# Kernel optimization log

Hardware: AMD Instinct MI355X
Metric: run time of the kernel (lower is better)

The kernel has to match this reference:

```python
import jax, jax.numpy as jnp
import numpy as np

B, S, D, F, E = 4, 2048, 512, 2048, 8  # batch, seq, d_model, d_ff, n_experts


def setup_inputs() -> dict:
    key = jax.random.key(0)
    k = jax.random.split(key, 5)
    x = jax.random.normal(k[0], (B, S, D), dtype=jnp.float32)
    Ws = jax.random.normal(k[1], (D, E), dtype=jnp.float32) * 0.02  # router weight
    bs = jnp.zeros((E,), dtype=jnp.float32)
    W1 = jax.random.normal(k[2], (E, D, F), dtype=jnp.float32) * 0.02
    b1 = jnp.zeros((E, F), dtype=jnp.float32)
    W2 = jax.random.normal(k[3], (E, F, D), dtype=jnp.float32) * 0.02
    b2 = jnp.zeros((E, D), dtype=jnp.float32)
    return {"x": x, "Ws": Ws, "bs": bs, "W1": W1, "b1": b1, "W2": W2, "b2": b2}


def reference(x, Ws, bs, W1, b1, W2, b2):
    # x: [B, S, D]. The torch module permutes in and permutes back, so the
    # batch/seq layout is preserved end to end; flatten to tokens [T, D].
    Bb, Ss, Dd = x.shape
    xt = x.reshape(-1, Dd)                       # [T, D]
    logits = xt @ Ws + bs                        # [T, E]
    probs = jax.nn.softmax(logits, axis=-1)
    prob_max = jnp.max(probs, axis=-1)           # [T] top-1 routing prob
    routes = jnp.argmax(probs, axis=-1)          # [T] expert ids
    onehot = jax.nn.one_hot(routes, W1.shape[0], dtype=xt.dtype)  # [T, E]

    # Per-expert FFN (eval mode: dropout is identity). drop_tokens=False, so
    # every token is processed by its routed expert. Dense dispatch: each
    # expert runs on all tokens, combine selects the routed output per token.
    def expert_ffn(w1, bb1, w2, bb2):
        h = jax.nn.gelu(xt @ w1 + bb1, approximate=False)  # [T, F] exact GELU (nn.GELU default)
        return h @ w2 + bb2                                # [T, D]

    y = jax.vmap(expert_ffn)(W1, b1, W2, b2)     # [E, T, D]
    out = jnp.einsum("te,etd->td", onehot, y)    # combine (scatter of routed outputs)
    out = out * prob_max[:, None]                # is_scale_prob=True
    return out.reshape(Bb, Ss, Dd)
```

## Files before the change

kernel.cpp:

```cpp
#include <hip/hip_runtime.h>
#include <hip/hip_fp16.h>
#include <cmath>

#define Tn 8192
#define Dn 512
#define Fn 2048
#define En 8

typedef _Float16 f16x8 __attribute__((ext_vector_type(8)));
typedef _Float16 f16x4 __attribute__((ext_vector_type(4)));
typedef float f32x4 __attribute__((ext_vector_type(4)));

#define MAXTILES 136

__device__ __forceinline__ void gload16(const void* g, void* l) {
    __builtin_amdgcn_global_load_lds(
        (const __attribute__((address_space(1))) unsigned int*)g,
        (__attribute__((address_space(3))) unsigned int*)l, 16, 0, 0);
}

__device__ __forceinline__ float fast_gelu(float v) {
    float z = fabsf(v) * 0.70710678118654752f;
    float t = 1.0f / fmaf(0.3275911f, z, 1.0f);
    float p = t * fmaf(t, fmaf(t, fmaf(t, fmaf(t, 1.061405429f, -1.453152027f),
                                       1.421413741f), -0.284496736f), 0.254829592f);
    float e = __expf(-z * z);
    float erfa = fmaf(-p, e, 1.0f);
    float phi = 0.5f + copysignf(0.5f * erfa, v);
    return v * phi;
}

__global__ __launch_bounds__(256) void router_kernel(
    const float* __restrict__ x, const float* __restrict__ Ws,
    const float* __restrict__ bs, _Float16* __restrict__ x16,
    int* __restrict__ route, float* __restrict__ scale,
    int* __restrict__ poslocal, int* __restrict__ blockCounts)
{
    __shared__ int hist[8];
    const int tid = threadIdx.x;
    if (tid < 8) hist[tid] = 0;
    __syncthreads();

    const int lane = tid & 63;
    const int w = tid >> 6;
    const int tokBase = blockIdx.x * 32 + w * 8;

    float wreg[8][8];
#pragma unroll
    for (int j = 0; j < 4; ++j) {
        const float4* p = reinterpret_cast<const float4*>(Ws + (4 * lane + j) * En);
        float4 a = p[0], b = p[1];
        wreg[j][0] = a.x; wreg[j][1] = a.y; wreg[j][2] = a.z; wreg[j][3] = a.w;
        wreg[j][4] = b.x; wreg[j][5] = b.y; wreg[j][6] = b.z; wreg[j][7] = b.w;
    }
#pragma unroll
    for (int j = 0; j < 4; ++j) {
        const float4* p = reinterpret_cast<const float4*>(Ws + (256 + 4 * lane + j) * En);
        float4 a = p[0], b = p[1];
        wreg[4 + j][0] = a.x; wreg[4 + j][1] = a.y; wreg[4 + j][2] = a.z; wreg[4 + j][3] = a.w;
        wreg[4 + j][4] = b.x; wreg[4 + j][5] = b.y; wreg[4 + j][6] = b.z; wreg[4 + j][7] = b.w;
    }
    float bsv[8];
#pragma unroll
    for (int e = 0; e < 8; ++e) bsv[e] = bs[e];

    for (int it = 0; it < 8; ++it) {
        int t = tokBase + it;
        const float4* xr = reinterpret_cast<const float4*>(x + (size_t)t * Dn);
        float4 v0 = xr[lane];
        float4 v1 = xr[64 + lane];
        f16x4 h0, h1;
        h0[0] = (_Float16)v0.x; h0[1] = (_Float16)v0.y; h0[2] = (_Float16)v0.z; h0[3] = (_Float16)v0.w;
        h1[0] = (_Float16)v1.x; h1[1] = (_Float16)v1.y; h1[2] = (_Float16)v1.z; h1[3] = (_Float16)v1.w;
        *reinterpret_cast<f16x4*>(x16 + (size_t)t * Dn + 4 * lane) = h0;
        *reinterpret_cast<f16x4*>(x16 + (size_t)t * Dn + 256 + 4 * lane) = h1;

        float xv[8] = {v0.x, v0.y, v0.z, v0.w, v1.x, v1.y, v1.z, v1.w};
        float part[8];
#pragma unroll
        for (int e = 0; e < 8; ++e) part[e] = 0.f;
#pragma unroll
        for (int j = 0; j < 8; ++j)
#pragma unroll
            for (int e = 0; e < 8; ++e) part[e] = fmaf(xv[j], wreg[j][e], part[e]);
#pragma unroll
        for (int s = 32; s > 0; s >>= 1) {
#pragma unroll
            for (int e = 0; e < 8; ++e) part[e] += __shfl_xor(part[e], s);
        }
        if (lane == 0) {
            float lg[8];
            lg[0] = part[0] + bsv[0];
            float m = lg[0]; int am = 0;
#pragma unroll
            for (int e = 1; e < 8; ++e) {
                lg[e] = part[e] + bsv[e];
                if (lg[e] > m) { m = lg[e]; am = e; }
            }
            float sum = 0.f;
#pragma unroll
            for (int e = 0; e < 8; ++e) sum += expf(lg[e] - m);
            route[t] = am;
            scale[t] = 1.0f / sum;
            poslocal[t] = atomicAdd(&hist[am], 1);
        }
    }
    __syncthreads();
    if (tid < 8) blockCounts[blockIdx.x * 8 + tid] = hist[tid];
}

__global__ __launch_bounds__(256) void plan_kernel(
    const int* __restrict__ blockCounts,
    int* __restrict__ base,
    int* __restrict__ nTiles, int* __restrict__ tileExpert,
    int* __restrict__ tileBase, int* __restrict__ tileEnd)
{
    __shared__ int cnt[256 * 8];
    __shared__ int groupSum[32 * 8];
    __shared__ int groupBase[32 * 8];
    __shared__ int totals[8];
    __shared__ int offsets_s[8];
    const int tid = threadIdx.x;
    for (int i = tid; i < 2048; i += 256) cnt[i] = blockCounts[i];
    __syncthreads();
    const int e = tid & 7, g = tid >> 3;
    {
        int s = 0;
#pragma unroll
        for (int b = g * 8; b < g * 8 + 8; ++b) s += cnt[b * 8 + e];
        groupSum[g * 8 + e] = s;
    }
    __syncthreads();
    if (tid < 8) {
        int run = 0;
        for (int gg = 0; gg < 32; ++gg) {
            groupBase[gg * 8 + tid] = run;
            run += groupSum[gg * 8 + tid];
        }
        totals[tid] = run;
    }
    __syncthreads();
    if (tid == 0) {
        int off = 0, nt = 0;
        for (int ee = 0; ee < En; ++ee) {
            offsets_s[ee] = off;
            int c = totals[ee];
            int tiles = (c + 63) / 64;
            for (int r = 0; r < tiles; ++r) {
                tileExpert[nt] = ee;
                tileBase[nt] = off + r * 64;
                tileEnd[nt] = off + c;
                ++nt;
            }
            off += c;
        }
        *nTiles = nt;
    }
    __syncthreads();
    {
        int run = offsets_s[e] + groupBase[g * 8 + e];
#pragma unroll
        for (int b = g * 8; b < g * 8 + 8; ++b) {
            base[b * 8 + e] = run;
            run += cnt[b * 8 + e];
        }
    }
}

__global__ __launch_bounds__(256) void scatter_kernel(
    const int* __restrict__ route, const int* __restrict__ poslocal,
    const int* __restrict__ base, int* __restrict__ order)
{
    int t = blockIdx.x * 256 + threadIdx.x;
    if (t >= Tn) return;
    int e = route[t];
    int rb = t >> 5;
    order[base[rb * 8 + e] + poslocal[t]] = t;
}

__global__ __launch_bounds__(256) void transpose_cvt_kernel(
    const float* __restrict__ W1, const float* __restrict__ W2,
    _Float16* __restrict__ W1T, _Float16* __restrict__ W2T)
{
    __shared__ float tile[64][65];
    int bx = blockIdx.x;
    const float* in; _Float16* outp; int R, C, tR, tC;
    if (bx < 2048) {
        int e = bx >> 8, t = bx & 255;
        R = Dn; C = Fn; tR = t >> 5; tC = t & 31;
        in = W1 + (size_t)e * Dn * Fn;
        outp = W1T + (size_t)e * Dn * Fn;
    } else {
        int b2 = bx - 2048;
        int e = b2 >> 8, t = b2 & 255;
        R = Fn; C = Dn; tR = t >> 3; tC = t & 7;
        in = W2 + (size_t)e * Fn * Dn;
        outp = W2T + (size_t)e * Fn * Dn;
    }
    int r0 = tR * 64, c0 = tC * 64;
    int row = threadIdx.x >> 2, cq = threadIdx.x & 3;
#pragma unroll
    for (int i = 0; i < 4; ++i) {
        float4 v = *reinterpret_cast<const float4*>(in + (size_t)(r0 + row) * C + c0 + cq * 16 + i * 4);
        tile[row][cq * 16 + i * 4 + 0] = v.x;
        tile[row][cq * 16 + i * 4 + 1] = v.y;
        tile[row][cq * 16 + i * 4 + 2] = v.z;
        tile[row][cq * 16 + i * 4 + 3] = v.w;
    }
    __syncthreads();
    int col = threadIdx.x >> 2, rq = threadIdx.x & 3;
    f16x8 o0, o1;
#pragma unroll
    for (int i = 0; i < 8; ++i) o0[i] = (_Float16)tile[rq * 16 + i][col];
#pragma unroll
    for (int i = 0; i < 8; ++i) o1[i] = (_Float16)tile[rq * 16 + 8 + i][col];
    size_t base = (size_t)(c0 + col) * R + r0 + rq * 16;
    *reinterpret_cast<f16x8*>(outp + base) = o0;
    *reinterpret_cast<f16x8*>(outp + base + 8) = o1;
}

__global__ __launch_bounds__(64) void gemm1_kernel(
    const _Float16* __restrict__ x16, const _Float16* __restrict__ W1T,
    const float* __restrict__ b1, const int* __restrict__ order,
    const int* __restrict__ nTiles, const int* __restrict__ tileExpert,
    const int* __restrict__ tileBase, const int* __restrict__ tileEnd,
    _Float16* __restrict__ hbuf)
{
    __shared__ _Float16 As[64 * 64];
    __shared__ _Float16 Bs[64 * 64];
    const int bx = blockIdx.x;
    const int bt = (bx & 7) * 17 + (bx >> 3);
    if (bt >= *nTiles) return;
    const int e = tileExpert[bt], rowBase = tileBase[bt], rowEnd = tileEnd[bt];
    const int nBase = blockIdx.y * 64;
    const int lane = threadIdx.x;

    const int swc = ((lane & 7) ^ (lane >> 3)) * 8;
    const _Float16* Asrc[8];
    const _Float16* Bsrc[8];
#pragma unroll
    for (int p = 0; p < 8; ++p) {
        int r = p * 8 + (lane >> 3);
        int tok = order[min(rowBase + r, Tn - 1)];
        Asrc[p] = x16 + (size_t)tok * Dn + swc;
        Bsrc[p] = W1T + (size_t)e * Dn * Fn + (size_t)(nBase + r) * Dn + swc;
    }

#define STAGE1(kt) do {                                                  \
        _Pragma("unroll")                                                \
        for (int p = 0; p < 8; ++p) {                                    \
            gload16(Asrc[p] + (kt) * 64, As + (p * 64 + lane) * 8);      \
            gload16(Bsrc[p] + (kt) * 64, Bs + (p * 64 + lane) * 8);      \
        }                                                                \
    } while (0)

    const int fr = lane & 15;
    const int off0 = (((lane >> 4))     ^ (lane & 7)) * 8;
    const int off1 = ((4 + (lane >> 4)) ^ (lane & 7)) * 8;

    f32x4 acc[4][4];
#pragma unroll
    for (int m = 0; m < 4; ++m)
#pragma unroll
        for (int n = 0; n < 4; ++n) acc[m][n] = {0.f, 0.f, 0.f, 0.f};

    STAGE1(0);
    const int NKT = Dn / 64;
    for (int kt = 0; kt < NKT; ++kt) {
        asm volatile("s_waitcnt vmcnt(0)" ::: "memory");
        f16x8 af[4][2], bf[4][2];
#pragma unroll
        for (int m = 0; m < 4; ++m) {
            af[m][0] = *reinterpret_cast<const f16x8*>(As + (m * 16 + fr) * 64 + off0);
            af[m][1] = *reinterpret_cast<const f16x8*>(As + (m * 16 + fr) * 64 + off1);
        }
#pragma unroll
        for (int n = 0; n < 4; ++n) {
            bf[n][0] = *reinterpret_cast<const f16x8*>(Bs + (n * 16 + fr) * 64 + off0);
            bf[n][1] = *reinterpret_cast<const f16x8*>(Bs + (n * 16 + fr) * 64 + off1);
        }
        asm volatile("s_waitcnt lgkmcnt(0)" ::: "memory");
        if (kt + 1 < NKT) STAGE1(kt + 1);
        __builtin_amdgcn_s_setprio(1);
#pragma unroll
        for (int ks = 0; ks < 2; ++ks)
#pragma unroll
            for (int m = 0; m < 4; ++m)
#pragma unroll
                for (int n = 0; n < 4; ++n)
                    acc[m][n] = __builtin_amdgcn_mfma_f32_16x16x32_f16(af[m][ks], bf[n][ks], acc[m][n], 0, 0, 0);
        __builtin_amdgcn_s_setprio(0);
    }
#undef STAGE1

    float b1v[4];
#pragma unroll
    for (int n = 0; n < 4; ++n) b1v[n] = b1[(size_t)e * Fn + nBase + n * 16 + fr];
#pragma unroll
    for (int m = 0; m < 4; ++m) {
#pragma unroll
        for (int j = 0; j < 4; ++j) {
            int i = rowBase + m * 16 + (lane >> 4) * 4 + j;
            if (i < rowEnd) {
#pragma unroll
                for (int n = 0; n < 4; ++n) {
                    float g = fast_gelu(acc[m][n][j] + b1v[n]);
                    hbuf[(size_t)i * Fn + nBase + n * 16 + fr] = (_Float16)g;
                }
            }
        }
    }
}

__global__ __launch_bounds__(64) void gemm2_kernel(
    const _Float16* __restrict__ hbuf, const _Float16* __restrict__ W2T,
    const float* __restrict__ b2, const int* __restrict__ order,
    const float* __restrict__ scale,
    const int* __restrict__ nTiles, const int* __restrict__ tileExpert,
    const int* __restrict__ tileBase, const int* __restrict__ tileEnd,
    float* __restrict__ out)
{
    __shared__ _Float16 As[64 * 64];
    __shared__ _Float16 Bs[32 * 64];
    const int bx = blockIdx.x;
    const int bt = (bx & 7) * 17 + (bx >> 3);
    if (bt >= *nTiles) return;
    const int e = tileExpert[bt], rowBase = tileBase[bt], rowEnd = tileEnd[bt];
    const int nBase = blockIdx.y * 32;
    const int lane = threadIdx.x;

    const int swc = ((lane & 7) ^ (lane >> 3)) * 8;
    const _Float16* Asrc[8];
    const _Float16* Bsrc[4];
#pragma unroll
    for (int p = 0; p < 8; ++p) {
        int r = p * 8 + (lane >> 3);
        Asrc[p] = hbuf + (size_t)min(rowBase + r, Tn - 1) * Fn + swc;
    }
#pragma unroll
    for (int p = 0; p < 4; ++p) {
        int r = p * 8 + (lane >> 3);
        Bsrc[p] = W2T + (size_t)e * Fn * Dn + (size_t)(nBase + r) * Fn + swc;
    }

#define STAGE2(kt) do {                                                  \
        _Pragma("unroll")                                                \
        for (int p = 0; p < 8; ++p)                                      \
            gload16(Asrc[p] + (kt) * 64, As + (p * 64 + lane) * 8);      \
        _Pragma("unroll")                                                \
        for (int p = 0; p < 4; ++p)                                      \
            gload16(Bsrc[p] + (kt) * 64, Bs + (p * 64 + lane) * 8);      \
    } while (0)

    const int fr = lane & 15;
    const int off0 = (((lane >> 4))     ^ (lane & 7)) * 8;
    const int off1 = ((4 + (lane >> 4)) ^ (lane & 7)) * 8;

    f32x4 acc[4][2];
#pragma unroll
    for (int m = 0; m < 4; ++m)
#pragma unroll
        for (int n = 0; n < 2; ++n) acc[m][n] = {0.f, 0.f, 0.f, 0.f};

    STAGE2(0);
    const int NKT = Fn / 64;
    for (int kt = 0; kt < NKT; ++kt) {
        asm volatile("s_waitcnt vmcnt(0)" ::: "memory");
        f16x8 af[4][2], bf[2][2];
#pragma unroll
        for (int m = 0; m < 4; ++m) {
            af[m][0] = *reinterpret_cast<const f16x8*>(As + (m * 16 + fr) * 64 + off0);
            af[m][1] = *reinterpret_cast<const f16x8*>(As + (m * 16 + fr) * 64 + off1);
        }
#pragma unroll
        for (int n = 0; n < 2; ++n) {
            bf[n][0] = *reinterpret_cast<const f16x8*>(Bs + (n * 16 + fr) * 64 + off0);
            bf[n][1] = *reinterpret_cast<const f16x8*>(Bs + (n * 16 + fr) * 64 + off1);
        }
        asm volatile("s_waitcnt lgkmcnt(0)" ::: "memory");
        if (kt + 1 < NKT) STAGE2(kt + 1);
        __builtin_amdgcn_s_setprio(1);
#pragma unroll
        for (int ks = 0; ks < 2; ++ks)
#pragma unroll
            for (int m = 0; m < 4; ++m)
#pragma unroll
                for (int n = 0; n < 2; ++n)
                    acc[m][n] = __builtin_amdgcn_mfma_f32_16x16x32_f16(af[m][ks], bf[n][ks], acc[m][n], 0, 0, 0);
        __builtin_amdgcn_s_setprio(0);
    }
#undef STAGE2

    float b2v[2];
#pragma unroll
    for (int n = 0; n < 2; ++n) b2v[n] = b2[(size_t)e * Dn + nBase + n * 16 + fr];
#pragma unroll
    for (int m = 0; m < 4; ++m) {
#pragma unroll
        for (int j = 0; j < 4; ++j) {
            int i = rowBase + m * 16 + (lane >> 4) * 4 + j;
            if (i < rowEnd) {
                int tok = order[i];
                float s = scale[tok];
#pragma unroll
                for (int n = 0; n < 2; ++n)
                    out[(size_t)tok * Dn + nBase + n * 16 + fr] = (acc[m][n][j] + b2v[n]) * s;
            }
        }
    }
}

extern "C" void kernel_launch(void* const* d_in, const int* in_sizes, int n_in,
                              void* d_out, int out_size, void* d_ws, size_t ws_size,
                              hipStream_t stream) {
    const float* x  = (const float*)d_in[0];
    const float* Ws = (const float*)d_in[1];
    const float* bs = (const float*)d_in[2];
    const float* W1 = (const float*)d_in[3];
    const float* b1 = (const float*)d_in[4];
    const float* W2 = (const float*)d_in[5];
    const float* b2 = (const float*)d_in[6];
    float* out = (float*)d_out;

    char* ws = (char*)d_ws;
    int* nTiles      = (int*)(ws + 0);
    int* tileExpert  = (int*)(ws + 256);
    int* tileBase    = (int*)(ws + 1024);
    int* tileEnd     = (int*)(ws + 2048);
    int* route       = (int*)(ws + 4096);
    float* scale     = (float*)(ws + 4096 + 4 * Tn);
    int* poslocal    = (int*)(ws + 4096 + 8 * Tn);
    int* order       = (int*)(ws + 4096 + 12 * Tn);
    int* blockCounts = (int*)(ws + 4096 + 16 * Tn);
    int* base        = (int*)(ws + 4096 + 16 * Tn + 8192);
    _Float16* x16    = (_Float16*)(ws + (1 << 20));
    _Float16* W1T    = x16 + (size_t)Tn * Dn;
    _Float16* W2T    = W1T + (size_t)En * Dn * Fn;
    _Float16* hbuf   = W2T + (size_t)En * Fn * Dn;

    router_kernel<<<256, 256, 0, stream>>>(x, Ws, bs, x16, route, scale, poslocal, blockCounts);
    plan_kernel<<<1, 256, 0, stream>>>(blockCounts, base, nTiles, tileExpert, tileBase, tileEnd);
    scatter_kernel<<<Tn / 256, 256, 0, stream>>>(route, poslocal, base, order);
    transpose_cvt_kernel<<<4096, 256, 0, stream>>>(W1, W2, W1T, W2T);
    gemm1_kernel<<<dim3(MAXTILES, Fn / 64), 64, 0, stream>>>(
        x16, W1T, b1, order, nTiles, tileExpert, tileBase, tileEnd, hbuf);
    gemm2_kernel<<<dim3(MAXTILES, Dn / 32), 64, 0, stream>>>(
        hbuf, W2T, b2, order, scale, nTiles, tileExpert, tileBase, tileEnd, out);
}
```

Before: 129.0 us.

## Merge router with weight transpose and widen gemm2 N tile to 64

Folds the router and the weight transpose/convert into one prep kernel launch, with block index selecting the role. This removes a launch and lets the two independent workloads share the GPU. Separately, gemm2 now computes a 64x64 output tile per block instead of 64x32, which halves the number of times the A (hbuf) tile is reloaded. The cost is more accumulator registers per thread and fewer blocks in the gemm2 grid.

```diff
diff --git a/kernel.cpp b/kernel.cpp
--- a/kernel.cpp
+++ b/kernel.cpp
@@ -30,83 +30,125 @@
     return v * phi;
 }
 
-__global__ __launch_bounds__(256) void router_kernel(
+__global__ __launch_bounds__(256) void prep_kernel(
     const float* __restrict__ x, const float* __restrict__ Ws,
     const float* __restrict__ bs, _Float16* __restrict__ x16,
     int* __restrict__ route, float* __restrict__ scale,
-    int* __restrict__ poslocal, int* __restrict__ blockCounts)
+    int* __restrict__ poslocal, int* __restrict__ blockCounts,
+    const float* __restrict__ W1, const float* __restrict__ W2,
+    _Float16* __restrict__ W1T, _Float16* __restrict__ W2T)
 {
+    __shared__ float tilebuf[64][65];
     __shared__ int hist[8];
     const int tid = threadIdx.x;
-    if (tid < 8) hist[tid] = 0;
+
+    if (blockIdx.x < 256) {
+        if (tid < 8) hist[tid] = 0;
+        __syncthreads();
+
+        const int lane = tid & 63;
+        const int w = tid >> 6;
+        const int tokBase = blockIdx.x * 32 + w * 8;
+
+        float wreg[8][8];
+#pragma unroll
+        for (int j = 0; j < 4; ++j) {
+            const float4* p = reinterpret_cast<const float4*>(Ws + (4 * lane + j) * En);
+            float4 a = p[0], b = p[1];
+            wreg[j][0] = a.x; wreg[j][1] = a.y; wreg[j][2] = a.z; wreg[j][3] = a.w;
+            wreg[j][4] = b.x; wreg[j][5] = b.y; wreg[j][6] = b.z; wreg[j][7] = b.w;
+        }
+#pragma unroll
+        for (int j = 0; j < 4; ++j) {
+            const float4* p = reinterpret_cast<const float4*>(Ws + (256 + 4 * lane + j) * En);
+            float4 a = p[0], b = p[1];
+            wreg[4 + j][0] = a.x; wreg[4 + j][1] = a.y; wreg[4 + j][2] = a.z; wreg[4 + j][3] = a.w;
+            wreg[4 + j][4] = b.x; wreg[4 + j][5] = b.y; wreg[4 + j][6] = b.z; wreg[4 + j][7] = b.w;
+        }
+        float bsv[8];
+#pragma unroll
+        for (int e = 0; e < 8; ++e) bsv[e] = bs[e];
+
+        for (int it = 0; it < 8; ++it) {
+            int t = tokBase + it;
+            const float4* xr = reinterpret_cast<const float4*>(x + (size_t)t * Dn);
+            float4 v0 = xr[lane];
+            float4 v1 = xr[64 + lane];
+            f16x4 h0, h1;
+            h0[0] = (_Float16)v0.x; h0[1] = (_Float16)v0.y; h0[2] = (_Float16)v0.z; h0[3] = (_Float16)v0.w;
+            h1[0] = (_Float16)v1.x; h1[1] = (_Float16)v1.y; h1[2] = (_Float16)v1.z; h1[3] = (_Float16)v1.w;
+            *reinterpret_cast<f16x4*>(x16 + (size_t)t * Dn + 4 * lane) = h0;
+            *reinterpret_cast<f16x4*>(x16 + (size_t)t * Dn + 256 + 4 * lane) = h1;
+
+            float xv[8] = {v0.x, v0.y, v0.z, v0.w, v1.x, v1.y, v1.z, v1.w};
+            float part[8];
+#pragma unroll
+            for (int e = 0; e < 8; ++e) part[e] = 0.f;
+#pragma unroll
+            for (int j = 0; j < 8; ++j)
+#pragma unroll
+                for (int e = 0; e < 8; ++e) part[e] = fmaf(xv[j], wreg[j][e], part[e]);
+#pragma unroll
+            for (int s = 32; s > 0; s >>= 1) {
+#pragma unroll
+                for (int e = 0; e < 8; ++e) part[e] += __shfl_xor(part[e], s);
+            }
+            if (lane == 0) {
+                float lg[8];
+                lg[0] = part[0] + bsv[0];
+                float m = lg[0]; int am = 0;
+#pragma unroll
+                for (int e = 1; e < 8; ++e) {
+                    lg[e] = part[e] + bsv[e];
+                    if (lg[e] > m) { m = lg[e]; am = e; }
+                }
+                float sum = 0.f;
+#pragma unroll
+                for (int e = 0; e < 8; ++e) sum += expf(lg[e] - m);
+                route[t] = am;
+                scale[t] = 1.0f / sum;
+                poslocal[t] = atomicAdd(&hist[am], 1);
+            }
+        }
+        __syncthreads();
+        if (tid < 8) blockCounts[blockIdx.x * 8 + tid] = hist[tid];
+        return;
+    }
+
+    int bx = blockIdx.x - 256;
+    const float* in; _Float16* outp; int R, C, tR, tC;
+    if (bx < 2048) {
+        int e = bx >> 8, t = bx & 255;
+        R = Dn; C = Fn; tR = t >> 5; tC = t & 31;
+        in = W1 + (size_t)e * Dn * Fn;
+        outp = W1T + (size_t)e * Dn * Fn;
+    } else {
+        int b2 = bx - 2048;
+        int e = b2 >> 8, t = b2 & 255;
+        R = Fn; C = Dn; tR = t >> 3; tC = t & 7;
+        in = W2 + (size_t)e * Fn * Dn;
+        outp = W2T + (size_t)e * Fn * Dn;
+    }
+    int r0 = tR * 64, c0 = tC * 64;
+    int row = tid >> 2, cq = tid & 3;
+#pragma unroll
+    for (int i = 0; i < 4; ++i) {
+        float4 v = *reinterpret_cast<const float4*>(in + (size_t)(r0 + row) * C + c0 + cq * 16 + i * 4);
+        tilebuf[row][cq * 16 + i * 4 + 0] = v.x;
+        tilebuf[row][cq * 16 + i * 4 + 1] = v.y;
+        tilebuf[row][cq * 16 + i * 4 + 2] = v.z;
+        tilebuf[row][cq * 16 + i * 4 + 3] = v.w;
+    }
     __syncthreads();
-
-    const int lane = tid & 63;
-    const int w = tid >> 6;
-    const int tokBase = blockIdx.x * 32 + w * 8;
-
-    float wreg[8][8];
-#pragma unroll
-    for (int j = 0; j < 4; ++j) {
-        const float4* p = reinterpret_cast<const float4*>(Ws + (4 * lane + j) * En);
-        float4 a = p[0], b = p[1];
-        wreg[j][0] = a.x; wreg[j][1] = a.y; wreg[j][2] = a.z; wreg[j][3] = a.w;
-        wreg[j][4] = b.x; wreg[j][5] = b.y; wreg[j][6] = b.z; wreg[j][7] = b.w;
-    }
-#pragma unroll
-    for (int j = 0; j < 4; ++j) {
-        const float4* p = reinterpret_cast<const float4*>(Ws + (256 + 4 * lane + j) * En);
-        float4 a = p[0], b = p[1];
-        wreg[4 + j][0] = a.x; wreg[4 + j][1] = a.y; wreg[4 + j][2] = a.z; wreg[4 + j][3] = a.w;
-        wreg[4 + j][4] = b.x; wreg[4 + j][5] = b.y; wreg[4 + j][6] = b.z; wreg[4 + j][7] = b.w;
-    }
-    float bsv[8];
-#pragma unroll
-    for (int e = 0; e < 8; ++e) bsv[e] = bs[e];
-
-    for (int it = 0; it < 8; ++it) {
-        int t = tokBase + it;
-        const float4* xr = reinterpret_cast<const float4*>(x + (size_t)t * Dn);
-        float4 v0 = xr[lane];
-        float4 v1 = xr[64 + lane];
-        f16x4 h0, h1;
-        h0[0] = (_Float16)v0.x; h0[1] = (_Float16)v0.y; h0[2] = (_Float16)v0.z; h0[3] = (_Float16)v0.w;
-        h1[0] = (_Float16)v1.x; h1[1] = (_Float16)v1.y; h1[2] = (_Float16)v1.z; h1[3] = (_Float16)v1.w;
-        *reinterpret_cast<f16x4*>(x16 + (size_t)t * Dn + 4 * lane) = h0;
-        *reinterpret_cast<f16x4*>(x16 + (size_t)t * Dn + 256 + 4 * lane) = h1;
-
-        float xv[8] = {v0.x, v0.y, v0.z, v0.w, v1.x, v1.y, v1.z, v1.w};
-        float part[8];
-#pragma unroll
-        for (int e = 0; e < 8; ++e) part[e] = 0.f;
-#pragma unroll
-        for (int j = 0; j < 8; ++j)
-#pragma unroll
-            for (int e = 0; e < 8; ++e) part[e] = fmaf(xv[j], wreg[j][e], part[e]);
-#pragma unroll
-        for (int s = 32; s > 0; s >>= 1) {
-#pragma unroll
-            for (int e = 0; e < 8; ++e) part[e] += __shfl_xor(part[e], s);
-        }
-        if (lane == 0) {
-            float lg[8];
-            lg[0] = part[0] + bsv[0];
-            float m = lg[0]; int am = 0;
-#pragma unroll
-            for (int e = 1; e < 8; ++e) {
-                lg[e] = part[e] + bsv[e];
-                if (lg[e] > m) { m = lg[e]; am = e; }
-            }
-            float sum = 0.f;
-#pragma unroll
-            for (int e = 0; e < 8; ++e) sum += expf(lg[e] - m);
-            route[t] = am;
-            scale[t] = 1.0f / sum;
-            poslocal[t] = atomicAdd(&hist[am], 1);
-        }
-    }
-    __syncthreads();
-    if (tid < 8) blockCounts[blockIdx.x * 8 + tid] = hist[tid];
+    int col = tid >> 2, rq = tid & 3;
+    f16x8 o0, o1;
+#pragma unroll
+    for (int i = 0; i < 8; ++i) o0[i] = (_Float16)tilebuf[rq * 16 + i][col];
+#pragma unroll
+    for (int i = 0; i < 8; ++i) o1[i] = (_Float16)tilebuf[rq * 16 + 8 + i][col];
+    size_t base = (size_t)(c0 + col) * R + r0 + rq * 16;
+    *reinterpret_cast<f16x8*>(outp + base) = o0;
+    *reinterpret_cast<f16x8*>(outp + base + 8) = o1;
 }
 
 __global__ __launch_bounds__(256) void plan_kernel(
@@ -178,47 +220,6 @@
     order[base[rb * 8 + e] + poslocal[t]] = t;
 }
 
-__global__ __launch_bounds__(256) void transpose_cvt_kernel(
-    const float* __restrict__ W1, const float* __restrict__ W2,
-    _Float16* __restrict__ W1T, _Float16* __restrict__ W2T)
-{
-    __shared__ float tile[64][65];
-    int bx = blockIdx.x;
-    const float* in; _Float16* outp; int R, C, tR, tC;
-    if (bx < 2048) {
-        int e = bx >> 8, t = bx & 255;
-        R = Dn; C = Fn; tR = t >> 5; tC = t & 31;
-        in = W1 + (size_t)e * Dn * Fn;
-        outp = W1T + (size_t)e * Dn * Fn;
-    } else {
-        int b2 = bx - 2048;
-        int e = b2 >> 8, t = b2 & 255;
-        R = Fn; C = Dn; tR = t >> 3; tC = t & 7;
-        in = W2 + (size_t)e * Fn * Dn;
-        outp = W2T + (size_t)e * Fn * Dn;
-    }
-    int r0 = tR * 64, c0 = tC * 64;
-    int row = threadIdx.x >> 2, cq = threadIdx.x & 3;
-#pragma unroll
-    for (int i = 0; i < 4; ++i) {
-        float4 v = *reinterpret_cast<const float4*>(in + (size_t)(r0 + row) * C + c0 + cq * 16 + i * 4);
-        tile[row][cq * 16 + i * 4 + 0] = v.x;
-        tile[row][cq * 16 + i * 4 + 1] = v.y;
-        tile[row][cq * 16 + i * 4 + 2] = v.z;
-        tile[row][cq * 16 + i * 4 + 3] = v.w;
-    }
-    __syncthreads();
-    int col = threadIdx.x >> 2, rq = threadIdx.x & 3;
-    f16x8 o0, o1;
-#pragma unroll
-    for (int i = 0; i < 8; ++i) o0[i] = (_Float16)tile[rq * 16 + i][col];
-#pragma unroll
-    for (int i = 0; i < 8; ++i) o1[i] = (_Float16)tile[rq * 16 + 8 + i][col];
-    size_t base = (size_t)(c0 + col) * R + r0 + rq * 16;
-    *reinterpret_cast<f16x8*>(outp + base) = o0;
-    *reinterpret_cast<f16x8*>(outp + base + 8) = o1;
-}
-
 __global__ __launch_bounds__(64) void gemm1_kernel(
     const _Float16* __restrict__ x16, const _Float16* __restrict__ W1T,
     const float* __restrict__ b1, const int* __restrict__ order,
@@ -321,59 +322,54 @@
     float* __restrict__ out)
 {
     __shared__ _Float16 As[64 * 64];
-    __shared__ _Float16 Bs[32 * 64];
+    __shared__ _Float16 Bs[64 * 64];
     const int bx = blockIdx.x;
     const int bt = (bx & 7) * 17 + (bx >> 3);
     if (bt >= *nTiles) return;
     const int e = tileExpert[bt], rowBase = tileBase[bt], rowEnd = tileEnd[bt];
-    const int nBase = blockIdx.y * 32;
+    const int nBase = blockIdx.y * 64;
     const int lane = threadIdx.x;
 
     const int swc = ((lane & 7) ^ (lane >> 3)) * 8;
     const _Float16* Asrc[8];
-    const _Float16* Bsrc[4];
+    const _Float16* Bsrc[8];
 #pragma unroll
     for (int p = 0; p < 8; ++p) {
         int r = p * 8 + (lane >> 3);
         Asrc[p] = hbuf + (size_t)min(rowBase + r, Tn - 1) * Fn + swc;
-    }
-#pragma unroll
-    for (int p = 0; p < 4; ++p) {
-        int r = p * 8 + (lane >> 3);
         Bsrc[p] = W2T + (size_t)e * Fn * Dn + (size_t)(nBase + r) * Fn + swc;
     }
 
 #define STAGE2(kt) do {                                                  \
         _Pragma("unroll")                                                \
-        for (int p = 0; p < 8; ++p)                                      \
+        for (int p = 0; p < 8; ++p) {                                    \
             gload16(Asrc[p] + (kt) * 64, As + (p * 64 + lane) * 8);      \
-        _Pragma("unroll")                                                \
-        for (int p = 0; p < 4; ++p)                                      \
             gload16(Bsrc[p] + (kt) * 64, Bs + (p * 64 + lane) * 8);      \
+        }                                                                \
     } while (0)
 
     const int fr = lane & 15;
     const int off0 = (((lane >> 4))     ^ (lane & 7)) * 8;
     const int off1 = ((4 + (lane >> 4)) ^ (lane & 7)) * 8;
 
-    f32x4 acc[4][2];
+    f32x4 acc[4][4];
 #pragma unroll
     for (int m = 0; m < 4; ++m)
 #pragma unroll
-        for (int n = 0; n < 2; ++n) acc[m][n] = {0.f, 0.f, 0.f, 0.f};
+        for (int n = 0; n < 4; ++n) acc[m][n] = {0.f, 0.f, 0.f, 0.f};
 
     STAGE2(0);
     const int NKT = Fn / 64;
     for (int kt = 0; kt < NKT; ++kt) {
         asm volatile("s_waitcnt vmcnt(0)" ::: "memory");
-        f16x8 af[4][2], bf[2][2];
+        f16x8 af[4][2], bf[4][2];
 #pragma unroll
         for (int m = 0; m < 4; ++m) {
             af[m][0] = *reinterpret_cast<const f16x8*>(As + (m * 16 + fr) * 64 + off0);
             af[m][1] = *reinterpret_cast<const f16x8*>(As + (m * 16 + fr) * 64 + off1);
         }
 #pragma unroll
-        for (int n = 0; n < 2; ++n) {
+        for (int n = 0; n < 4; ++n) {
             bf[n][0] = *reinterpret_cast<const f16x8*>(Bs + (n * 16 + fr) * 64 + off0);
             bf[n][1] = *reinterpret_cast<const f16x8*>(Bs + (n * 16 + fr) * 64 + off1);
         }
@@ -385,15 +381,15 @@
 #pragma unroll
             for (int m = 0; m < 4; ++m)
 #pragma unroll
-                for (int n = 0; n < 2; ++n)
+                for (int n = 0; n < 4; ++n)
                     acc[m][n] = __builtin_amdgcn_mfma_f32_16x16x32_f16(af[m][ks], bf[n][ks], acc[m][n], 0, 0, 0);
         __builtin_amdgcn_s_setprio(0);
     }
 #undef STAGE2
 
-    float b2v[2];
-#pragma unroll
-    for (int n = 0; n < 2; ++n) b2v[n] = b2[(size_t)e * Dn + nBase + n * 16 + fr];
+    float b2v[4];
+#pragma unroll
+    for (int n = 0; n < 4; ++n) b2v[n] = b2[(size_t)e * Dn + nBase + n * 16 + fr];
 #pragma unroll
     for (int m = 0; m < 4; ++m) {
 #pragma unroll
@@ -403,7 +399,7 @@
                 int tok = order[i];
                 float s = scale[tok];
 #pragma unroll
-                for (int n = 0; n < 2; ++n)
+                for (int n = 0; n < 4; ++n)
                     out[(size_t)tok * Dn + nBase + n * 16 + fr] = (acc[m][n][j] + b2v[n]) * s;
             }
         }
@@ -438,12 +434,12 @@
     _Float16* W2T    = W1T + (size_t)En * Dn * Fn;
     _Float16* hbuf   = W2T + (size_t)En * Fn * Dn;
 
-    router_kernel<<<256, 256, 0, stream>>>(x, Ws, bs, x16, route, scale, poslocal, blockCounts);
+    prep_kernel<<<256 + 4096, 256, 0, stream>>>(x, Ws, bs, x16, route, scale, poslocal,
+                                                blockCounts, W1, W2, W1T, W2T);
     plan_kernel<<<1, 256, 0, stream>>>(blockCounts, base, nTiles, tileExpert, tileBase, tileEnd);
     scatter_kernel<<<Tn / 256, 256, 0, stream>>>(route, poslocal, base, order);
-    transpose_cvt_kernel<<<4096, 256, 0, stream>>>(W1, W2, W1T, W2T);
     gemm1_kernel<<<dim3(MAXTILES, Fn / 64), 64, 0, stream>>>(
         x16, W1T, b1, order, nTiles, tileExpert, tileBase, tileEnd, hbuf);
-    gemm2_kernel<<<dim3(MAXTILES, Dn / 32), 64, 0, stream>>>(
+    gemm2_kernel<<<dim3(MAXTILES, Dn / 64), 64, 0, stream>>>(
         hbuf, W2T, b2, order, scale, nTiles, tileExpert, tileBase, tileEnd, out);
 }
```

Measured after the change: 112.2 us. -13.0%, faster.
